# Kernel optimization log

Measured on AMD Instinct MI355X. Metric: run time of the kernel, lower is better.

The kernel has to match this reference:

```python
import jax, jax.numpy as jnp
import numpy as np

N_FEATURES = 8  # hardcoded chain length in the original call()


def setup_inputs() -> dict:
    key = jax.random.key(0)
    k1, k2 = jax.random.split(key)
    B, F, D, R, U = 512, N_FEATURES, 4, 32, 64
    X = jax.random.normal(k1, (B, F, D), dtype=jnp.float32)
    # kernel: [local_dim, rank, rank, n_features, units]; scale ~0.1 keeps the
    # 8-step matmul chain numerically O(1)
    kernel = jax.random.normal(k2, (D, R, R, F, U), dtype=jnp.float32) * 0.1
    return {"X": X, "kernel": kernel}


def reference(X, kernel):
    # X: [B, F=8, D]; kernel: [D, R, R, F, U]
    # Per unit u and feature f: T_f[b] = sum_d X[b,f,d] * kernel[d,:,:,f,u]  (R x R)
    # output[b,u] = trace(T_0 @ T_1 @ ... @ T_7)
    # Vectorized over all units at once; chain of 7 batched matmuls.
    M = jnp.einsum('bd,dijfu->buij', X[:, 0, :], kernel[:, :, :, 0:1, :])  # [B,U,R,R]
    for f in range(1, N_FEATURES):
        T = jnp.einsum('bd,dijfu->buij', X[:, f, :], kernel[:, :, :, f:f+1, :])
        M = jnp.einsum('buij,bujk->buik', M, T)
    return jnp.einsum('buii->bu', M)  # trace -> [B, U]; activation is identity
```

## Files before the change

kernel.cpp:

```cpp
#include <hip/hip_runtime.h>
#include <hip/hip_fp16.h>

#define NB 512
#define NF 8
#define ND 4
#define NR 32
#define NU 64
#define G  4

typedef float f32x4 __attribute__((ext_vector_type(4)));
typedef unsigned u32x4 __attribute__((ext_vector_type(4)));
typedef _Float16 f16x8 __attribute__((ext_vector_type(8)));

__device__ inline unsigned pkmul_h(unsigned a, unsigned s) {
    unsigned d;
    asm("v_pk_mul_f16 %0, %1, %2" : "=v"(d) : "v"(a), "s"(s));
    return d;
}
__device__ inline unsigned pkfma_h(unsigned a, unsigned s, unsigned c) {
    unsigned d;
    asm("v_pk_fma_f16 %0, %1, %2, %3" : "=v"(d) : "v"(a), "s"(s), "v"(c));
    return d;
}

__device__ inline unsigned pkrtz(float a, float b) {
    auto h = __builtin_amdgcn_cvt_pkrtz(a, b);
    static_assert(sizeof(h) == 4, "cvt_pkrtz must return 32-bit");
    return __builtin_bit_cast(unsigned, h);
}

__device__ inline unsigned h2pack(float a, float b) {
    unsigned ha = (unsigned)__half_as_ushort(__float2half(a));
    unsigned hb = (unsigned)__half_as_ushort(__float2half(b));
    return ha | (hb << 16);
}

__device__ inline unsigned rfl_u(unsigned v) {
    return (unsigned)__builtin_amdgcn_readfirstlane((int)v);
}

__global__ __launch_bounds__(256) void tr_k3h(const float* __restrict__ K,
                                              unsigned* __restrict__ K3h) {
    __shared__ float lds[256 * 36];
    const int t   = threadIdx.x;
    const int bid = blockIdx.x;
    const int uh = bid & 1, jp = (bid >> 1) & 3, q = (bid >> 3) & 3, f = bid >> 5;
    const int u0 = uh * 32;

    {
        const int rr = t >> 3, col4 = (t & 7) * 4;
#pragma unroll
        for (int i = 0; i < 8; ++i) {
            int r = i * 32 + rr;
            int d = r >> 6, s = r & 63;
            int e = q * 256 + jp * 64 + s;
            f32x4 v = *(const f32x4*)(K + ((size_t)((d << 10) + e) << 9)
                                        + (f << 6) + u0 + col4);
            *(f32x4*)(lds + r * 36 + col4) = v;
        }
    }
    __syncthreads();
    {
        const int u_l = t >> 3, lane8 = t & 7;
        unsigned* dst = K3h + ((size_t)((u0 + u_l) * 8 + f) << 11)
                            + ((q * 4 + jp) << 7);
#pragma unroll
        for (int g2 = 0; g2 < 8; ++g2) {
            int idx4 = lane8 + g2 * 8;
            int dh = idx4 & 1, Ic = idx4 >> 1;
            int d0 = dh * 2;
            float v0 = lds[(d0 * 64 + 0  + Ic) * 36 + u_l];
            float v1 = lds[(d0 * 64 + 32 + Ic) * 36 + u_l];
            float v2 = lds[((d0 + 1) * 64 + 0  + Ic) * 36 + u_l];
            float v3 = lds[((d0 + 1) * 64 + 32 + Ic) * 36 + u_l];
            uint2 wv; wv.x = h2pack(v0, v1); wv.y = h2pack(v2, v3);
            *(uint2*)(dst + idx4 * 2) = wv;
        }
    }
}

__global__ __launch_bounds__(128)
__attribute__((amdgpu_waves_per_eu(4, 4)))
void tr_main14(const float* __restrict__ X,
               const unsigned* __restrict__ K3h,
               float* __restrict__ out) {
    const int tid  = threadIdx.x;
    const int w    = __builtin_amdgcn_readfirstlane(tid >> 6);
    const int lane = tid & 63;
    const int c    = lane & 15;
    const int q    = lane >> 4;
    const int u      = blockIdx.x & 63;
    const int bgroup = blockIdx.x >> 6;
    const int b0     = ((bgroup << 1) + w) * G;

    __shared__ __attribute__((aligned(16))) char lds[2 * G * 2048];
    char* Nb0 = lds + w * (G * 2048);

    f16x8 idf0, idf1;
#pragma unroll
    for (int jj = 0; jj < 8; ++jj) {
        idf0[jj] = (8 * q + jj == c) ? (_Float16)1.0f : (_Float16)0.0f;
        idf1[jj] = (8 * q + jj == 16 + c) ? (_Float16)1.0f : (_Float16)0.0f;
    }

    const unsigned* Kt = K3h + ((size_t)u << 14) + (q << 9) + (c << 2);
    const f32x4 z = {0.f, 0.f, 0.f, 0.f};

#pragma unroll
    for (int f = 0; f < NF; ++f) {
        const unsigned* Kf = Kt + (f << 11);

        unsigned xdd[G][4];
#pragma unroll
        for (int g = 0; g < G; ++g) {
            const f32x4 xv = *(const f32x4*)(X + ((b0 + g) << 5) + (f << 2));
#pragma unroll
            for (int d = 0; d < 4; ++d)
                xdd[g][d] = rfl_u(pkrtz(xv[d], xv[d]));
        }

        u32x4 A0u[G], A1u[G];
        u32x4 s0 = *(const u32x4*)(Kf + 0);
        u32x4 s1 = *(const u32x4*)(Kf + 64);
#pragma unroll
        for (int jp = 0; jp < 4; ++jp) {
            u32x4 c0 = s0, c1 = s1;
            if (jp < 3) {
                const unsigned* pn = Kf + ((jp + 1) << 7);
                s0 = *(const u32x4*)(pn + 0);
                s1 = *(const u32x4*)(pn + 64);
            }
#pragma unroll
            for (int g = 0; g < G; ++g) {
                {
                    unsigned tv = pkmul_h(c0[0], xdd[g][0]);
                    tv = pkfma_h(c0[1], xdd[g][1], tv);
                    tv = pkfma_h(c0[2], xdd[g][2], tv);
                    tv = pkfma_h(c0[3], xdd[g][3], tv);
                    A0u[g][jp] = tv;
                }
                {
                    unsigned tv = pkmul_h(c1[0], xdd[g][0]);
                    tv = pkfma_h(c1[1], xdd[g][1], tv);
                    tv = pkfma_h(c1[2], xdd[g][2], tv);
                    tv = pkfma_h(c1[3], xdd[g][3], tv);
                    A1u[g][jp] = tv;
                }
            }
        }

#pragma unroll
        for (int g = 0; g < G; ++g) {
            char* nb = Nb0 + (g << 11);
            f16x8 A0 = __builtin_bit_cast(f16x8, A0u[g]);
            f16x8 A1 = __builtin_bit_cast(f16x8, A1u[g]);

            f16x8 bf0, bf1;
            if (f == 0) { bf0 = idf0; bf1 = idf1; }
            else {
                bf0 = *(const f16x8*)(nb + (((q << 5) | c) << 4));
                bf1 = *(const f16x8*)(nb + (((q << 5) | c) << 4) + 256);
            }

            if (f < NF - 1) {
                f32x4 c00 = __builtin_amdgcn_mfma_f32_16x16x32_f16(A0, bf0, z, 0, 0, 0);
                f32x4 c01 = __builtin_amdgcn_mfma_f32_16x16x32_f16(A0, bf1, z, 0, 0, 0);
                f32x4 c10 = __builtin_amdgcn_mfma_f32_16x16x32_f16(A1, bf0, z, 0, 0, 0);
                f32x4 c11 = __builtin_amdgcn_mfma_f32_16x16x32_f16(A1, bf1, z, 0, 0, 0);
#pragma unroll
                for (int I = 0; I < 2; ++I)
#pragma unroll
                    for (int J = 0; J < 2; ++J) {
                        f32x4 a = (I == 0) ? (J == 0 ? c00 : c01)
                                           : (J == 0 ? c10 : c11);
                        unsigned lo = pkrtz(a[0], a[1]);
                        unsigned hi = pkrtz(a[2], a[3]);
                        uint2 val; val.x = lo; val.y = hi;
                        *(uint2*)(nb + (((((I << 1) | (q >> 1)) << 5) | (J << 4) | c) << 4)
                                     + ((q & 1) << 3)) = val;
                    }
            } else {
                f32x4 c00 = __builtin_amdgcn_mfma_f32_16x16x32_f16(A0, bf0, z, 0, 0, 0);
                f32x4 c11 = __builtin_amdgcn_mfma_f32_16x16x32_f16(A1, bf1, z, 0, 0, 0);
                f32x4 t4 = c00 + c11;
                int ri = c & 3;
                float s = (ri == 0) ? t4[0] : (ri == 1) ? t4[1]
                        : (ri == 2) ? t4[2] : t4[3];
                s = ((c >> 2) == q) ? s : 0.f;
#pragma unroll
                for (int m = 32; m >= 1; m >>= 1) s += __shfl_xor(s, m, 64);
                if (lane == 0) out[((b0 + g) << 6) + u] = s;
            }
        }
        asm volatile("" ::: "memory");
    }
}

extern "C" void kernel_launch(void* const* d_in, const int* in_sizes, int n_in,
                              void* d_out, int out_size, void* d_ws, size_t ws_size,
                              hipStream_t stream) {
    (void)in_sizes; (void)n_in; (void)out_size; (void)ws_size;
    const float* X = (const float*)d_in[0];
    const float* K = (const float*)d_in[1];
    float* out = (float*)d_out;
    unsigned* K3h = (unsigned*)d_ws;

    hipLaunchKernelGGL(tr_k3h, dim3(256), dim3(256), 0, stream, K, K3h);
    hipLaunchKernelGGL(tr_main14, dim3(4096), dim3(128), 0, stream, X, K3h, out);
}
```

Before: 95.43 us.

## Pre-pack X to half in prep kernel and prefetch next feature's K slice

The prep kernel now also converts X into packed fp16 pairs in extra workspace, so the main kernel loads ready-made operands instead of converting and calling readfirstlane. The K transpose uses twice as many, smaller blocks (16 units each) to spread that work more widely. In the main loop, the first K fragment of the next feature is prefetched during the last jp step, so global load latency overlaps across feature boundaries. The cost is an extra workspace buffer, a slightly larger prep launch and more live registers in the main kernel.

New measurement: 95.32 us. Within noise of the previous version (-0.1%).

```diff
diff --git a/kernel.cpp b/kernel.cpp
--- a/kernel.cpp
+++ b/kernel.cpp
@@ -35,44 +35,57 @@
     return ha | (hb << 16);
 }
 
-__device__ inline unsigned rfl_u(unsigned v) {
-    return (unsigned)__builtin_amdgcn_readfirstlane((int)v);
-}
-
-__global__ __launch_bounds__(256) void tr_k3h(const float* __restrict__ K,
-                                              unsigned* __restrict__ K3h) {
-    __shared__ float lds[256 * 36];
+__global__ __launch_bounds__(256) void tr_k3h16(const float* __restrict__ K,
+                                                const float* __restrict__ X,
+                                                unsigned* __restrict__ K3h,
+                                                unsigned* __restrict__ Xh) {
+    __shared__ float lds[256 * 20];
     const int t   = threadIdx.x;
     const int bid = blockIdx.x;
-    const int uh = bid & 1, jp = (bid >> 1) & 3, q = (bid >> 3) & 3, f = bid >> 5;
-    const int u0 = uh * 32;
+
+    if (bid >= 512) {
+        const int tt = (bid - 512) * 256 + t;
+#pragma unroll
+        for (int k = 0; k < 4; ++k) {
+            int pair = tt * 4 + k;
+            const f32x4 xv = *(const f32x4*)(X + pair * 4);
+            u32x4 wv;
+#pragma unroll
+            for (int d = 0; d < 4; ++d) wv[d] = pkrtz(xv[d], xv[d]);
+            *(u32x4*)(Xh + pair * 4) = wv;
+        }
+        return;
+    }
+
+    const int uq = bid & 3, jp = (bid >> 2) & 3, q = (bid >> 4) & 3, f = bid >> 6;
+    const int u0 = uq * 16;
 
     {
-        const int rr = t >> 3, col4 = (t & 7) * 4;
-#pragma unroll
-        for (int i = 0; i < 8; ++i) {
-            int r = i * 32 + rr;
+        const int rr = t >> 2, col4 = (t & 3) * 4;
+#pragma unroll
+        for (int i = 0; i < 4; ++i) {
+            int r = i * 64 + rr;
             int d = r >> 6, s = r & 63;
             int e = q * 256 + jp * 64 + s;
             f32x4 v = *(const f32x4*)(K + ((size_t)((d << 10) + e) << 9)
                                         + (f << 6) + u0 + col4);
-            *(f32x4*)(lds + r * 36 + col4) = v;
+            *(f32x4*)(lds + r * 20 + col4) = v;
         }
     }
     __syncthreads();
     {
-        const int u_l = t >> 3, lane8 = t & 7;
+        const int u_l = t >> 4, lane16 = t & 15;
         unsigned* dst = K3h + ((size_t)((u0 + u_l) * 8 + f) << 11)
                             + ((q * 4 + jp) << 7);
 #pragma unroll
-        for (int g2 = 0; g2 < 8; ++g2) {
-            int idx4 = lane8 + g2 * 8;
+        for (int g2 = 0; g2 < 4; ++g2) {
+            int idx4 = lane16 + g2 * 16;
             int dh = idx4 & 1, Ic = idx4 >> 1;
             int d0 = dh * 2;
-            float v0 = lds[(d0 * 64 + 0  + Ic) * 36 + u_l];
-            float v1 = lds[(d0 * 64 + 32 + Ic) * 36 + u_l];
-            float v2 = lds[((d0 + 1) * 64 + 0  + Ic) * 36 + u_l];
-            float v3 = lds[((d0 + 1) * 64 + 32 + Ic) * 36 + u_l];
+            float v0 = lds[(d0 * 64 + 0  + Ic) * 20 + u_l];
+            float v1 = lds[(d0 * 64 + 32 + Ic) * 20 + u_l];
+            float v2 = lds[((d0 + 1) * 64 + 0  + Ic) * 20 + u_l];
+            float v3 = lds[((d0 + 1) * 64 + 32 + Ic) * 20 + u_l];
             uint2 wv; wv.x = h2pack(v0, v1); wv.y = h2pack(v2, v3);
             *(uint2*)(dst + idx4 * 2) = wv;
         }
@@ -81,7 +94,7 @@
 
 __global__ __launch_bounds__(128)
 __attribute__((amdgpu_waves_per_eu(4, 4)))
-void tr_main14(const float* __restrict__ X,
+void tr_main16(const unsigned* __restrict__ Xh,
                const unsigned* __restrict__ K3h,
                float* __restrict__ out) {
     const int tid  = threadIdx.x;
@@ -106,27 +119,28 @@
     const unsigned* Kt = K3h + ((size_t)u << 14) + (q << 9) + (c << 2);
     const f32x4 z = {0.f, 0.f, 0.f, 0.f};
 
+    u32x4 s0 = *(const u32x4*)(Kt + 0);
+    u32x4 s1 = *(const u32x4*)(Kt + 64);
+
 #pragma unroll
     for (int f = 0; f < NF; ++f) {
         const unsigned* Kf = Kt + (f << 11);
 
-        unsigned xdd[G][4];
-#pragma unroll
-        for (int g = 0; g < G; ++g) {
-            const f32x4 xv = *(const f32x4*)(X + ((b0 + g) << 5) + (f << 2));
-#pragma unroll
-            for (int d = 0; d < 4; ++d)
-                xdd[g][d] = rfl_u(pkrtz(xv[d], xv[d]));
-        }
+        u32x4 xdd[G];
+#pragma unroll
+        for (int g = 0; g < G; ++g)
+            xdd[g] = *(const u32x4*)(Xh + ((b0 + g) << 5) + (f << 2));
 
         u32x4 A0u[G], A1u[G];
-        u32x4 s0 = *(const u32x4*)(Kf + 0);
-        u32x4 s1 = *(const u32x4*)(Kf + 64);
 #pragma unroll
         for (int jp = 0; jp < 4; ++jp) {
             u32x4 c0 = s0, c1 = s1;
             if (jp < 3) {
                 const unsigned* pn = Kf + ((jp + 1) << 7);
+                s0 = *(const u32x4*)(pn + 0);
+                s1 = *(const u32x4*)(pn + 64);
+            } else if (f < NF - 1) {
+                const unsigned* pn = Kf + 2048;
                 s0 = *(const u32x4*)(pn + 0);
                 s1 = *(const u32x4*)(pn + 64);
             }
@@ -204,7 +218,8 @@
     const float* K = (const float*)d_in[1];
     float* out = (float*)d_out;
     unsigned* K3h = (unsigned*)d_ws;
-
-    hipLaunchKernelGGL(tr_k3h, dim3(256), dim3(256), 0, stream, K, K3h);
-    hipLaunchKernelGGL(tr_main14, dim3(4096), dim3(128), 0, stream, X, K3h, out);
-}
+    unsigned* Xh  = (unsigned*)((char*)d_ws + (4u << 20));
+
+    hipLaunchKernelGGL(tr_k3h16, dim3(516), dim3(256), 0, stream, K, X, K3h, Xh);
+    hipLaunchKernelGGL(tr_main16, dim3(4096), dim3(128), 0, stream, Xh, K3h, out);
+}
```
